# Performance work log

Hardware: AMD Instinct MI355X
Metric: run time of the kernel (lower is better)

The kernel has to match this reference:

```python
import jax, jax.numpy as jnp
import numpy as np
from jax import lax

B, S, H, T = 64, 512, 1024, 24


def setup_inputs() -> dict:
    key = jax.random.key(0)
    k1, k2, k3, k4, k5 = jax.random.split(key, 5)
    feats = jax.random.normal(k1, (B, S, H), dtype=jnp.float32)
    target = jax.random.randint(k2, (B, S), 0, T)  # tag ids (argmax of original one-hot target)
    # descending-sorted lengths -> prefix mask, matching the torch code's sorted-batch assumption
    lengths = jnp.sort(jax.random.randint(k3, (B,), S // 2, S + 1))[::-1]
    mask = jnp.arange(S)[None, :] < lengths[:, None]  # (B,S) bool
    # hidden2tag params (uniform init ~ nn.Linear default scale)
    bound = 1.0 / np.sqrt(H)
    W = jax.random.uniform(k4, (T, H), minval=-bound, maxval=bound, dtype=jnp.float32)
    b = jax.random.uniform(k5, (T,), minval=-bound, maxval=bound, dtype=jnp.float32)
    transition = jnp.zeros((T, T), dtype=jnp.float32)
    return {"feats": feats, "target": target, "mask": mask, "W": W, "b": b, "transition": transition}


def reference(feats, target, mask, W, b, transition):
    # emission scores: (B,S,T)
    emission = jnp.einsum("bsh,th->bst", feats, W) + b
    # gold path score
    sc = jnp.take_along_axis(emission, target[:, :, None], axis=2).squeeze(-1)  # (B,S)
    sc = sc.at[:, 1:].add(transition[target[:, :-1], target[:, 1:]])
    total_score = (sc * mask.astype(emission.dtype)).sum(axis=1)  # (B,)
    # forward algorithm (log-partition) as a scan over time
    p0 = emission[:, 0]  # (B,T)
    emis_t = jnp.swapaxes(emission[:, 1:], 0, 1)  # (S-1,B,T)
    mask_t = jnp.swapaxes(mask[:, 1:], 0, 1)      # (S-1,B)

    def step(p, xs):
        emit_i, m_i = xs
        # log_sum[b, prev, cur] = p[b, prev] + transition[prev, cur] + emit_i[b, cur]
        new_p = jax.nn.logsumexp(p[:, :, None] + transition[None, :, :] + emit_i[:, None, :], axis=1)
        return jnp.where(m_i[:, None], new_p, p), None

    p, _ = lax.scan(step, p0, (emis_t, mask_t))
    log_Z = jax.nn.logsumexp(p, axis=1)  # (B,)
    loss = -jnp.mean(total_score - log_Z)
    return loss, emission
```

## Files before the change

kernel.cpp:

```cpp
#include <hip/hip_runtime.h>
#include <cstdint>
#include <math.h>

#define B_ 64
#define S_ 512
#define H_ 1024
#define T_ 24
#define TP_ 32
#define NC_ 32
#define CL_ 16
#define KST_ 1040

typedef unsigned int u32;
typedef unsigned short u16;
typedef __attribute__((ext_vector_type(8))) short short8v;
typedef __attribute__((ext_vector_type(4))) float f32x4;
typedef __attribute__((ext_vector_type(4))) u32 uint4v;

__device__ __forceinline__ float rl_f32(float x, int sl) {
    return __uint_as_float(__builtin_amdgcn_readlane(__float_as_uint(x), sl));
}

__device__ __forceinline__ void split_pk(float f0, float f1, u32& hpk, u32& lpk) {
    const u32 u0 = __float_as_uint(f0), u1 = __float_as_uint(f1);
    const u32 t1 = u1 & 0xffff0000u;
    hpk = (u0 >> 16) | t1;
    const float fl0 = f0 - __uint_as_float(u0 & 0xffff0000u);
    const float fl1 = f1 - __uint_as_float(t1);
    lpk = (__float_as_uint(fl0) >> 16) | (__float_as_uint(fl1) & 0xffff0000u);
}

__global__ __launch_bounds__(256) void wcvt_kernel(const float* __restrict__ W,
                                                   u16* __restrict__ Wh,
                                                   u16* __restrict__ Wl,
                                                   float* __restrict__ out) {
    const int i = blockIdx.x * 256 + threadIdx.x;
    if (i == 0) out[0] = 0.f;
    const int t = i >> 10;
    const float f = (t < T_) ? W[i] : 0.f;
    const u32 u = __float_as_uint(f);
    const u32 rh = u + 0x7fffu + ((u >> 16) & 1u);
    const u16 hb = (u16)(rh >> 16);
    const float fh = __uint_as_float((u32)hb << 16);
    const float fl = f - fh;
    const u32 u2 = __float_as_uint(fl);
    const u32 rl2 = u2 + 0x7fffu + ((u2 >> 16) & 1u);
    Wh[i] = hb;
    Wl[i] = (u16)(rl2 >> 16);
}

__global__ __launch_bounds__(256) void gemm_kernel(const float* __restrict__ feats,
                                                   const u16* __restrict__ Wh,
                                                   const u16* __restrict__ Wl,
                                                   const float* __restrict__ bias,
                                                   float* __restrict__ emission) {
    const int tid  = threadIdx.x;
    const int lane = tid & 63;
    const int wv   = tid >> 6;
    const int r16  = lane & 15;
    const int g    = lane >> 4;
    const int mtile = blockIdx.x * 4 + wv;

    const float* ap  = feats + ((long)mtile * 16 + r16) * H_ + g * 8;
    const u16* bh0p = Wh + r16 * H_ + g * 8;
    const u16* bl0p = Wl + r16 * H_ + g * 8;
    const u16* bh1p = Wh + (r16 + 16) * H_ + g * 8;
    const u16* bl1p = Wl + (r16 + 16) * H_ + g * 8;

    f32x4 acc0 = {0.f, 0.f, 0.f, 0.f};
    f32x4 acc1 = {0.f, 0.f, 0.f, 0.f};

#pragma unroll 4
    for (int kk = 0; kk < H_ / 32; ++kk) {
        const int ko = kk * 32;
        const float4 a0 = *(const float4*)(ap + ko);
        const float4 a1 = *(const float4*)(ap + ko + 4);
        const short8v bh0 = *(const short8v*)(bh0p + ko);
        const short8v bl0 = *(const short8v*)(bl0p + ko);
        const short8v bh1 = *(const short8v*)(bh1p + ko);
        const short8v bl1 = *(const short8v*)(bl1p + ko);

        u32 h0, l0, h1, l1, h2, l2, h3, l3;
        split_pk(a0.x, a0.y, h0, l0);
        split_pk(a0.z, a0.w, h1, l1);
        split_pk(a1.x, a1.y, h2, l2);
        split_pk(a1.z, a1.w, h3, l3);
        const uint4v hv = {h0, h1, h2, h3};
        const uint4v lv = {l0, l1, l2, l3};
        const short8v ah = __builtin_bit_cast(short8v, hv);
        const short8v al = __builtin_bit_cast(short8v, lv);

        acc0 = __builtin_amdgcn_mfma_f32_16x16x32_bf16(al, bh0, acc0, 0, 0, 0);
        acc0 = __builtin_amdgcn_mfma_f32_16x16x32_bf16(ah, bl0, acc0, 0, 0, 0);
        acc0 = __builtin_amdgcn_mfma_f32_16x16x32_bf16(ah, bh0, acc0, 0, 0, 0);
        acc1 = __builtin_amdgcn_mfma_f32_16x16x32_bf16(al, bh1, acc1, 0, 0, 0);
        acc1 = __builtin_amdgcn_mfma_f32_16x16x32_bf16(ah, bl1, acc1, 0, 0, 0);
        acc1 = __builtin_amdgcn_mfma_f32_16x16x32_bf16(ah, bh1, acc1, 0, 0, 0);
    }

    const float b0 = bias[r16];
    const float b1 = (r16 + 16 < T_) ? bias[r16 + 16] : 0.f;
    float* op = emission + ((long)mtile * 16 + g * 4) * T_;
#pragma unroll
    for (int r = 0; r < 4; ++r) {
        op[r * T_ + r16] = acc0[r] + b0;
        if (r16 + 16 < T_) op[r * T_ + r16 + 16] = acc1[r] + b1;
    }
}

__global__ __launch_bounds__(64, 1) void chunk_kernel(const float* __restrict__ emission,
                                                      const int* __restrict__ mask,
                                                      const float* __restrict__ trans,
                                                      float* __restrict__ wsK) {
    __shared__ u32 lds[2][2][16][18];
    const int bid = blockIdx.x;
    const int c_ = bid & (NC_ - 1);
    const int b  = bid >> 5;
    const int l  = threadIdx.x;
    const int cc = l & 15;
    const int q  = l >> 4;
    const int aq4 = (l & 48);

    const float* em = emission + (long)b * S_ * T_;
    const int* mk = mask + b * S_;

    int mc = 0;
#pragma unroll
    for (int k = 0; k < 8; ++k) mc += mk[l + k * 64];
#pragma unroll
    for (int off = 32; off; off >>= 1) mc += __shfl_xor(mc, off);
    const int len = __builtin_amdgcn_readfirstlane(mc);

    const int lo = 1 + c_ * CL_;
    const int hi = min(lo + CL_, S_);
    const int send = min(hi, len);

    short8v Ah[2], Al[2];
#pragma unroll
    for (int I = 0; I < 2; ++I) {
        const int j = 16 * I + cc;
        u32 hw[4], lw[4];
#pragma unroll
        for (int w = 0; w < 4; ++w) {
            const int t0 = 8 * q + 2 * w;
            const float v0 = (t0 < 24 && j < 24) ? __expf(trans[t0 * T_ + j]) : 0.f;
            const float v1 = (t0 + 1 < 24 && j < 24) ? __expf(trans[(t0 + 1) * T_ + j]) : 0.f;
            split_pk(v0, v1, hw[w], lw[w]);
        }
        const uint4v hv = {hw[0], hw[1], hw[2], hw[3]};
        const uint4v lv = {lw[0], lw[1], lw[2], lw[3]};
        Ah[I] = __builtin_bit_cast(short8v, hv);
        Al[I] = __builtin_bit_cast(short8v, lv);
    }

    f32x4 K[2][2];
#pragma unroll
    for (int I = 0; I < 2; ++I)
#pragma unroll
        for (int J = 0; J < 2; ++J)
#pragma unroll
            for (int r = 0; r < 4; ++r)
                K[I][J][r] = (16 * I + 4 * q + r == 16 * J + cc) ? 1.f : 0.f;

    u32 bh[2][4], bl[2][4];
#pragma unroll
    for (int J = 0; J < 2; ++J)
#pragma unroll
        for (int w = 0; w < 4; ++w) {
            const int k0 = 8 * q + 2 * w, col = 16 * J + cc;
            bh[J][w] = (k0 == col ? 0x3f80u : 0u) | (k0 + 1 == col ? 0x3f800000u : 0u);
            bl[J][w] = 0u;
        }

    const int xj = ((l & 31) < 24) ? (l & 31) : 0;
    float xr_[CL_];
#pragma unroll
    for (int k = 0; k < CL_; ++k) {
        const int s = lo + k;
        xr_[k] = em[((s < S_) ? s : 0) * T_ + xj];
    }

    float Ls = 0.f;
    const f32x4 z4 = {0.f, 0.f, 0.f, 0.f};

#pragma unroll
    for (int k = 0; k < CL_; ++k) {
        const int s = lo + k;
        if (s < send) {
            const uint4v bh0v = {bh[0][0], bh[0][1], bh[0][2], bh[0][3]};
            const uint4v bh1v = {bh[1][0], bh[1][1], bh[1][2], bh[1][3]};
            const uint4v bl0v = {bl[0][0], bl[0][1], bl[0][2], bl[0][3]};
            const uint4v bl1v = {bl[1][0], bl[1][1], bl[1][2], bl[1][3]};
            const short8v B0h = __builtin_bit_cast(short8v, bh0v);
            const short8v B1h = __builtin_bit_cast(short8v, bh1v);
            const short8v B0l = __builtin_bit_cast(short8v, bl0v);
            const short8v B1l = __builtin_bit_cast(short8v, bl1v);

            f32x4 acc[2][2];
#pragma unroll
            for (int I = 0; I < 2; ++I) {
                acc[I][0] = __builtin_amdgcn_mfma_f32_16x16x32_bf16(Ah[I], B0h, z4, 0, 0, 0);
                acc[I][0] = __builtin_amdgcn_mfma_f32_16x16x32_bf16(Ah[I], B0l, acc[I][0], 0, 0, 0);
                acc[I][0] = __builtin_amdgcn_mfma_f32_16x16x32_bf16(Al[I], B0h, acc[I][0], 0, 0, 0);
                acc[I][1] = __builtin_amdgcn_mfma_f32_16x16x32_bf16(Ah[I], B1h, z4, 0, 0, 0);
                acc[I][1] = __builtin_amdgcn_mfma_f32_16x16x32_bf16(Ah[I], B1l, acc[I][1], 0, 0, 0);
                acc[I][1] = __builtin_amdgcn_mfma_f32_16x16x32_bf16(Al[I], B1h, acc[I][1], 0, 0, 0);
            }

            const float X = __expf(xr_[k]);
            const int xi = __float_as_int(X);
            float xr0[4], xr1[4];
#pragma unroll
            for (int r = 0; r < 4; ++r) {
                xr0[r] = __int_as_float(__builtin_amdgcn_ds_bpermute(aq4 + 4 * r, xi));
                xr1[r] = __int_as_float(__builtin_amdgcn_ds_bpermute(aq4 + 64 + 4 * r, xi));
            }
#pragma unroll
            for (int J = 0; J < 2; ++J)
#pragma unroll
                for (int r = 0; r < 4; ++r) {
                    K[0][J][r] = acc[0][J][r] * xr0[r];
                    K[1][J][r] = acc[1][J][r] * xr1[r];
                }

            if (k == 7 || k == CL_ - 1) {
                float mx = K[0][0][0];
#pragma unroll
                for (int I = 0; I < 2; ++I)
#pragma unroll
                    for (int J = 0; J < 2; ++J)
#pragma unroll
                        for (int r = 0; r < 4; ++r) mx = fmaxf(mx, K[I][J][r]);
#pragma unroll
                for (int off = 32; off; off >>= 1) mx = fmaxf(mx, __shfl_xor(mx, off));
                const u32 ef = __float_as_uint(mx) & 0x7f800000u;
                const float inv = __uint_as_float(0x7f000000u - ef);
#pragma unroll
                for (int I = 0; I < 2; ++I)
#pragma unroll
                    for (int J = 0; J < 2; ++J)
#pragma unroll
                        for (int r = 0; r < 4; ++r) K[I][J][r] *= inv;
                Ls += (float)((int)(ef >> 23) - 127) * 0.6931471805599453f;
            }

            if (k < CL_ - 1) {
#pragma unroll
                for (int I = 0; I < 2; ++I)
#pragma unroll
                    for (int J = 0; J < 2; ++J)
#pragma unroll
                        for (int m = 0; m < 2; ++m) {
                            u32 h, lo_w;
                            split_pk(K[I][J][2 * m], K[I][J][2 * m + 1], h, lo_w);
                            const int p = 8 * I + 2 * q + m;
                            lds[0][J][p][cc] = h;
                            lds[1][J][p][cc] = lo_w;
                        }
#pragma unroll
                for (int J = 0; J < 2; ++J)
#pragma unroll
                    for (int w = 0; w < 4; ++w) {
                        bh[J][w] = lds[0][J][4 * q + w][cc];
                        bl[J][w] = lds[1][J][4 * q + w][cc];
                    }
            }
        }
    }

    float* outp = wsK + (long)(b * NC_ + c_) * KST_;
#pragma unroll
    for (int I = 0; I < 2; ++I)
#pragma unroll
        for (int J = 0; J < 2; ++J)
#pragma unroll
            for (int r = 0; r < 4; ++r)
                outp[(16 * I + 4 * q + r) * 32 + 16 * J + cc] = K[I][J][r];
    if (l == 0) outp[1024] = Ls;
}

#define ACC4(kv, t0)                                                           \
    s0 = fmaf(rl_f32(p, (t0) + 0), kv.x, s0);                                  \
    s1 = fmaf(rl_f32(p, (t0) + 1), kv.y, s1);                                  \
    s2 = fmaf(rl_f32(p, (t0) + 2), kv.z, s2);                                  \
    s3 = fmaf(rl_f32(p, (t0) + 3), kv.w, s3);

__global__ __launch_bounds__(64) void finalize_kernel(const float* __restrict__ emission,
                                                      const int* __restrict__ target,
                                                      const int* __restrict__ mask,
                                                      const float* __restrict__ trans,
                                                      const float* __restrict__ wsK,
                                                      float* __restrict__ out) {
    const int b = blockIdx.x;
    const int j = threadIdx.x;
    const int jj = j < 24 ? j : 23;
    const float* em = emission + (long)b * S_ * T_;
    const int* mk = mask + b * S_;

    float p = (j < 24) ? __expf(em[j]) : 0.f;
    float C = 0.f;

    for (int c = 0; c < NC_; ++c) {
        const float* base = wsK + (long)(b * NC_ + c) * KST_;
        C += base[1024];
        const float4* rp = (const float4*)(base + jj * 32);
        const float4 k0 = rp[0], k1 = rp[1], k2 = rp[2], k3 = rp[3], k4 = rp[4], k5 = rp[5];
        float s0 = 0.f, s1 = 0.f, s2 = 0.f, s3 = 0.f;
        ACC4(k0, 0) ACC4(k1, 4) ACC4(k2, 8) ACC4(k3, 12) ACC4(k4, 16) ACC4(k5, 20)
        p = (j < 24) ? ((s0 + s1) + (s2 + s3)) : 0.f;
        float mx = p;
#pragma unroll
        for (int off = 32; off; off >>= 1) mx = fmaxf(mx, __shfl_xor(mx, off));
        const u32 ef = __float_as_uint(mx) & 0x7f800000u;
        p *= __uint_as_float(0x7f000000u - ef);
        C += (float)((int)(ef >> 23) - 127) * 0.6931471805599453f;
    }

    float ex = p;
#pragma unroll
    for (int off = 32; off; off >>= 1) ex += __shfl_down(ex, off);

    float ssum = 0.f;
#pragma unroll
    for (int kk = 0; kk < S_ / 64; ++kk) {
        const int s = j + kk * 64;
        if (mk[s]) {
            const int tg = target[b * S_ + s];
            float v = em[s * T_ + tg];
            if (s > 0) v += trans[target[b * S_ + s - 1] * T_ + tg];
            ssum += v;
        }
    }
#pragma unroll
    for (int off = 32; off; off >>= 1) ssum += __shfl_down(ssum, off);

    if (j == 0) {
        const float logZ = C + __logf(ex);
        atomicAdd(out, (logZ - ssum) * (1.0f / B_));
    }
}

extern "C" void kernel_launch(void* const* d_in, const int* in_sizes, int n_in,
                              void* d_out, int out_size, void* d_ws, size_t ws_size,
                              hipStream_t stream) {
    const float* feats  = (const float*)d_in[0];
    const int*   target = (const int*)d_in[1];
    const int*   mask   = (const int*)d_in[2];
    const float* W      = (const float*)d_in[3];
    const float* bias   = (const float*)d_in[4];
    const float* trans  = (const float*)d_in[5];

    float* out = (float*)d_out;
    float* emission = out + 1;
    u16* Wh = (u16*)d_ws;
    u16* Wl = Wh + TP_ * H_;
    float* wsK = (float*)((char*)d_ws + 131072);

    wcvt_kernel<<<(TP_ * H_) / 256, 256, 0, stream>>>(W, Wh, Wl, out);
    gemm_kernel<<<512, 256, 0, stream>>>(feats, Wh, Wl, bias, emission);
    chunk_kernel<<<B_ * NC_, 64, 0, stream>>>(emission, mask, trans, wsK);
    finalize_kernel<<<B_, 64, 0, stream>>>(emission, target, mask, trans, wsK, out);
}
```

Measured before the change: 260.0 us.

## Split GEMM K across waves and software-pipeline loads three stages deep

```diff
diff --git a/kernel.cpp b/kernel.cpp
--- a/kernel.cpp
+++ b/kernel.cpp
@@ -49,36 +49,62 @@
     Wl[i] = (u16)(rl2 >> 16);
 }
 
-__global__ __launch_bounds__(256) void gemm_kernel(const float* __restrict__ feats,
-                                                   const u16* __restrict__ Wh,
-                                                   const u16* __restrict__ Wl,
-                                                   const float* __restrict__ bias,
-                                                   float* __restrict__ emission) {
+__global__ __launch_bounds__(256, 4) void gemm_kernel(const float* __restrict__ feats,
+                                                      const u16* __restrict__ Wh,
+                                                      const u16* __restrict__ Wl,
+                                                      const float* __restrict__ bias,
+                                                      float* __restrict__ emission) {
+    __shared__ f32x4 ldsP[2][64][2];
     const int tid  = threadIdx.x;
     const int lane = tid & 63;
     const int wv   = tid >> 6;
+    const int mt_in = wv & 1;
+    const int kh    = wv >> 1;
     const int r16  = lane & 15;
     const int g    = lane >> 4;
-    const int mtile = blockIdx.x * 4 + wv;
-
-    const float* ap  = feats + ((long)mtile * 16 + r16) * H_ + g * 8;
-    const u16* bh0p = Wh + r16 * H_ + g * 8;
-    const u16* bl0p = Wl + r16 * H_ + g * 8;
-    const u16* bh1p = Wh + (r16 + 16) * H_ + g * 8;
-    const u16* bl1p = Wl + (r16 + 16) * H_ + g * 8;
+    const int mtile = blockIdx.x * 2 + mt_in;
+
+    const long ko0 = (long)kh * 512 + g * 8;
+    const float* ap  = feats + ((long)mtile * 16 + r16) * H_ + ko0;
+    const u16* bh0p = Wh + r16 * H_ + ko0;
+    const u16* bl0p = Wl + r16 * H_ + ko0;
+    const u16* bh1p = Wh + (r16 + 16) * H_ + ko0;
+    const u16* bl1p = Wl + (r16 + 16) * H_ + ko0;
 
     f32x4 acc0 = {0.f, 0.f, 0.f, 0.f};
     f32x4 acc1 = {0.f, 0.f, 0.f, 0.f};
 
-#pragma unroll 4
-    for (int kk = 0; kk < H_ / 32; ++kk) {
-        const int ko = kk * 32;
-        const float4 a0 = *(const float4*)(ap + ko);
-        const float4 a1 = *(const float4*)(ap + ko + 4);
-        const short8v bh0 = *(const short8v*)(bh0p + ko);
-        const short8v bl0 = *(const short8v*)(bl0p + ko);
-        const short8v bh1 = *(const short8v*)(bh1p + ko);
-        const short8v bl1 = *(const short8v*)(bl1p + ko);
+    float4 A0[3], A1[3];
+    short8v BH0[3], BL0[3], BH1[3], BL1[3];
+#pragma unroll
+    for (int p = 0; p < 3; ++p) {
+        const int ko = p * 32;
+        A0[p]  = *(const float4*)(ap + ko);
+        A1[p]  = *(const float4*)(ap + ko + 4);
+        BH0[p] = *(const short8v*)(bh0p + ko);
+        BL0[p] = *(const short8v*)(bl0p + ko);
+        BH1[p] = *(const short8v*)(bh1p + ko);
+        BL1[p] = *(const short8v*)(bl1p + ko);
+    }
+
+#pragma unroll
+    for (int kk = 0; kk < 16; ++kk) {
+        const int sl = kk % 3;
+        const float4 a0 = A0[sl];
+        const float4 a1 = A1[sl];
+        const short8v bh0 = BH0[sl];
+        const short8v bl0 = BL0[sl];
+        const short8v bh1 = BH1[sl];
+        const short8v bl1 = BL1[sl];
+        if (kk + 3 < 16) {
+            const int ko = (kk + 3) * 32;
+            A0[sl]  = *(const float4*)(ap + ko);
+            A1[sl]  = *(const float4*)(ap + ko + 4);
+            BH0[sl] = *(const short8v*)(bh0p + ko);
+            BL0[sl] = *(const short8v*)(bl0p + ko);
+            BH1[sl] = *(const short8v*)(bh1p + ko);
+            BL1[sl] = *(const short8v*)(bl1p + ko);
+        }
 
         u32 h0, l0, h1, l1, h2, l2, h3, l3;
         split_pk(a0.x, a0.y, h0, l0);
@@ -98,13 +124,27 @@
         acc1 = __builtin_amdgcn_mfma_f32_16x16x32_bf16(ah, bh1, acc1, 0, 0, 0);
     }
 
-    const float b0 = bias[r16];
-    const float b1 = (r16 + 16 < T_) ? bias[r16 + 16] : 0.f;
-    float* op = emission + ((long)mtile * 16 + g * 4) * T_;
-#pragma unroll
-    for (int r = 0; r < 4; ++r) {
-        op[r * T_ + r16] = acc0[r] + b0;
-        if (r16 + 16 < T_) op[r * T_ + r16 + 16] = acc1[r] + b1;
+    if (kh == 1) {
+        ldsP[mt_in][lane][0] = acc0;
+        ldsP[mt_in][lane][1] = acc1;
+    }
+    __syncthreads();
+    if (kh == 0) {
+        const f32x4 p0 = ldsP[mt_in][lane][0];
+        const f32x4 p1 = ldsP[mt_in][lane][1];
+#pragma unroll
+        for (int r = 0; r < 4; ++r) {
+            acc0[r] += p0[r];
+            acc1[r] += p1[r];
+        }
+        const float b0 = bias[r16];
+        const float b1 = (r16 + 16 < T_) ? bias[r16 + 16] : 0.f;
+        float* op = emission + ((long)mtile * 16 + g * 4) * T_;
+#pragma unroll
+        for (int r = 0; r < 4; ++r) {
+            op[r * T_ + r16] = acc0[r] + b0;
+            if (r16 + 16 < T_) op[r * T_ + r16 + 16] = acc1[r] + b1;
+        }
     }
 }
 
@@ -357,7 +397,7 @@
     float* wsK = (float*)((char*)d_ws + 131072);
 
     wcvt_kernel<<<(TP_ * H_) / 256, 256, 0, stream>>>(W, Wh, Wl, out);
-    gemm_kernel<<<512, 256, 0, stream>>>(feats, Wh, Wl, bias, emission);
+    gemm_kernel<<<1024, 256, 0, stream>>>(feats, Wh, Wl, bias, emission);
     chunk_kernel<<<B_ * NC_, 64, 0, stream>>>(emission, mask, trans, wsK);
     finalize_kernel<<<B_, 64, 0, stream>>>(emission, target, mask, trans, wsK, out);
 }
```

Result: no change. 259.0 us (-0.4%).

## Fuse emission GEMM, chunk scan and finalize into one kernel

Applied to the files above, without the earlier changes.

```diff
diff --git a/kernel.cpp b/kernel.cpp
--- a/kernel.cpp
+++ b/kernel.cpp
@@ -33,9 +33,11 @@
 __global__ __launch_bounds__(256) void wcvt_kernel(const float* __restrict__ W,
                                                    u16* __restrict__ Wh,
                                                    u16* __restrict__ Wl,
-                                                   float* __restrict__ out) {
+                                                   float* __restrict__ out,
+                                                   int* __restrict__ cnt) {
     const int i = blockIdx.x * 256 + threadIdx.x;
     if (i == 0) out[0] = 0.f;
+    if (i < B_) cnt[i] = 0;
     const int t = i >> 10;
     const float f = (t < T_) ? W[i] : 0.f;
     const u32 u = __float_as_uint(f);
@@ -49,70 +51,22 @@
     Wl[i] = (u16)(rl2 >> 16);
 }
 
-__global__ __launch_bounds__(256) void gemm_kernel(const float* __restrict__ feats,
-                                                   const u16* __restrict__ Wh,
-                                                   const u16* __restrict__ Wl,
-                                                   const float* __restrict__ bias,
-                                                   float* __restrict__ emission) {
-    const int tid  = threadIdx.x;
-    const int lane = tid & 63;
-    const int wv   = tid >> 6;
-    const int r16  = lane & 15;
-    const int g    = lane >> 4;
-    const int mtile = blockIdx.x * 4 + wv;
-
-    const float* ap  = feats + ((long)mtile * 16 + r16) * H_ + g * 8;
-    const u16* bh0p = Wh + r16 * H_ + g * 8;
-    const u16* bl0p = Wl + r16 * H_ + g * 8;
-    const u16* bh1p = Wh + (r16 + 16) * H_ + g * 8;
-    const u16* bl1p = Wl + (r16 + 16) * H_ + g * 8;
-
-    f32x4 acc0 = {0.f, 0.f, 0.f, 0.f};
-    f32x4 acc1 = {0.f, 0.f, 0.f, 0.f};
-
-#pragma unroll 4
-    for (int kk = 0; kk < H_ / 32; ++kk) {
-        const int ko = kk * 32;
-        const float4 a0 = *(const float4*)(ap + ko);
-        const float4 a1 = *(const float4*)(ap + ko + 4);
-        const short8v bh0 = *(const short8v*)(bh0p + ko);
-        const short8v bl0 = *(const short8v*)(bl0p + ko);
-        const short8v bh1 = *(const short8v*)(bh1p + ko);
-        const short8v bl1 = *(const short8v*)(bl1p + ko);
-
-        u32 h0, l0, h1, l1, h2, l2, h3, l3;
-        split_pk(a0.x, a0.y, h0, l0);
-        split_pk(a0.z, a0.w, h1, l1);
-        split_pk(a1.x, a1.y, h2, l2);
-        split_pk(a1.z, a1.w, h3, l3);
-        const uint4v hv = {h0, h1, h2, h3};
-        const uint4v lv = {l0, l1, l2, l3};
-        const short8v ah = __builtin_bit_cast(short8v, hv);
-        const short8v al = __builtin_bit_cast(short8v, lv);
-
-        acc0 = __builtin_amdgcn_mfma_f32_16x16x32_bf16(al, bh0, acc0, 0, 0, 0);
-        acc0 = __builtin_amdgcn_mfma_f32_16x16x32_bf16(ah, bl0, acc0, 0, 0, 0);
-        acc0 = __builtin_amdgcn_mfma_f32_16x16x32_bf16(ah, bh0, acc0, 0, 0, 0);
-        acc1 = __builtin_amdgcn_mfma_f32_16x16x32_bf16(al, bh1, acc1, 0, 0, 0);
-        acc1 = __builtin_amdgcn_mfma_f32_16x16x32_bf16(ah, bl1, acc1, 0, 0, 0);
-        acc1 = __builtin_amdgcn_mfma_f32_16x16x32_bf16(ah, bh1, acc1, 0, 0, 0);
-    }
-
-    const float b0 = bias[r16];
-    const float b1 = (r16 + 16 < T_) ? bias[r16 + 16] : 0.f;
-    float* op = emission + ((long)mtile * 16 + g * 4) * T_;
-#pragma unroll
-    for (int r = 0; r < 4; ++r) {
-        op[r * T_ + r16] = acc0[r] + b0;
-        if (r16 + 16 < T_) op[r * T_ + r16 + 16] = acc1[r] + b1;
-    }
-}
-
-__global__ __launch_bounds__(64, 1) void chunk_kernel(const float* __restrict__ emission,
+#define FINE_DECL(i) const float E##i##_ = 0.f; (void)E##i##_;
+
+__global__ __launch_bounds__(64, 1) void fused_kernel(const float* __restrict__ feats,
+                                                      const u16* __restrict__ Wh,
+                                                      const u16* __restrict__ Wl,
+                                                      const float* __restrict__ bias,
+                                                      const float* __restrict__ trans,
+                                                      const int* __restrict__ target,
                                                       const int* __restrict__ mask,
-                                                      const float* __restrict__ trans,
-                                                      float* __restrict__ wsK) {
+                                                      float* __restrict__ emission,
+                                                      float* __restrict__ wsK,
+                                                      int* __restrict__ cnt,
+                                                      float* __restrict__ out) {
+    __shared__ float em_lds[16][32];
     __shared__ u32 lds[2][2][16][18];
+
     const int bid = blockIdx.x;
     const int c_ = bid & (NC_ - 1);
     const int b  = bid >> 5;
@@ -124,6 +78,59 @@
     const float* em = emission + (long)b * S_ * T_;
     const int* mk = mask + b * S_;
 
+    {
+        const long row0 = (long)b * S_ + 16 * c_;
+        const float* ap  = feats + (row0 + cc) * H_ + q * 8;
+        const u16* bh0p = Wh + cc * H_ + q * 8;
+        const u16* bl0p = Wl + cc * H_ + q * 8;
+        const u16* bh1p = Wh + (cc + 16) * H_ + q * 8;
+        const u16* bl1p = Wl + (cc + 16) * H_ + q * 8;
+
+        f32x4 acc0 = {0.f, 0.f, 0.f, 0.f};
+        f32x4 acc1 = {0.f, 0.f, 0.f, 0.f};
+
+#pragma unroll 4
+        for (int kk = 0; kk < H_ / 32; ++kk) {
+            const int ko = kk * 32;
+            const float4 a0 = *(const float4*)(ap + ko);
+            const float4 a1 = *(const float4*)(ap + ko + 4);
+            const short8v bh0 = *(const short8v*)(bh0p + ko);
+            const short8v bl0 = *(const short8v*)(bl0p + ko);
+            const short8v bh1 = *(const short8v*)(bh1p + ko);
+            const short8v bl1 = *(const short8v*)(bl1p + ko);
+
+            u32 h0, l0, h1, l1, h2, l2, h3, l3;
+            split_pk(a0.x, a0.y, h0, l0);
+            split_pk(a0.z, a0.w, h1, l1);
+            split_pk(a1.x, a1.y, h2, l2);
+            split_pk(a1.z, a1.w, h3, l3);
+            const uint4v hv = {h0, h1, h2, h3};
+            const uint4v lv = {l0, l1, l2, l3};
+            const short8v ah = __builtin_bit_cast(short8v, hv);
+            const short8v al = __builtin_bit_cast(short8v, lv);
+
+            acc0 = __builtin_amdgcn_mfma_f32_16x16x32_bf16(al, bh0, acc0, 0, 0, 0);
+            acc0 = __builtin_amdgcn_mfma_f32_16x16x32_bf16(ah, bl0, acc0, 0, 0, 0);
+            acc0 = __builtin_amdgcn_mfma_f32_16x16x32_bf16(ah, bh0, acc0, 0, 0, 0);
+            acc1 = __builtin_amdgcn_mfma_f32_16x16x32_bf16(al, bh1, acc1, 0, 0, 0);
+            acc1 = __builtin_amdgcn_mfma_f32_16x16x32_bf16(ah, bl1, acc1, 0, 0, 0);
+            acc1 = __builtin_amdgcn_mfma_f32_16x16x32_bf16(ah, bh1, acc1, 0, 0, 0);
+        }
+
+        const float b0 = bias[cc];
+        const float b1 = (cc + 16 < T_) ? bias[cc + 16] : 0.f;
+#pragma unroll
+        for (int r = 0; r < 4; ++r) {
+            const float e0 = acc0[r] + b0;
+            const float e1 = acc1[r] + b1;
+            em_lds[4 * q + r][cc] = e0;
+            em_lds[4 * q + r][16 + cc] = e1;
+            float* op = emission + (row0 + 4 * q + r) * T_;
+            op[cc] = e0;
+            if (cc + 16 < T_) op[16 + cc] = e1;
+        }
+    }
+
     int mc = 0;
 #pragma unroll
     for (int k = 0; k < 8; ++k) mc += mk[l + k * 64];
@@ -131,9 +138,8 @@
     for (int off = 32; off; off >>= 1) mc += __shfl_xor(mc, off);
     const int len = __builtin_amdgcn_readfirstlane(mc);
 
-    const int lo = 1 + c_ * CL_;
-    const int hi = min(lo + CL_, S_);
-    const int send = min(hi, len);
+    const int s0_ = 16 * c_;
+    const int send = min(s0_ + CL_, len);
 
     short8v Ah[2], Al[2];
 #pragma unroll
@@ -172,21 +178,13 @@
             bl[J][w] = 0u;
         }
 
-    const int xj = ((l & 31) < 24) ? (l & 31) : 0;
-    float xr_[CL_];
-#pragma unroll
-    for (int k = 0; k < CL_; ++k) {
-        const int s = lo + k;
-        xr_[k] = em[((s < S_) ? s : 0) * T_ + xj];
-    }
-
     float Ls = 0.f;
     const f32x4 z4 = {0.f, 0.f, 0.f, 0.f};
 
 #pragma unroll
     for (int k = 0; k < CL_; ++k) {
-        const int s = lo + k;
-        if (s < send) {
+        const int s = s0_ + k;
+        if (s > 0 && s < send) {
             const uint4v bh0v = {bh[0][0], bh[0][1], bh[0][2], bh[0][3]};
             const uint4v bh1v = {bh[1][0], bh[1][1], bh[1][2], bh[1][3]};
             const uint4v bl0v = {bl[0][0], bl[0][1], bl[0][2], bl[0][3]};
@@ -207,7 +205,7 @@
                 acc[I][1] = __builtin_amdgcn_mfma_f32_16x16x32_bf16(Al[I], B1h, acc[I][1], 0, 0, 0);
             }
 
-            const float X = __expf(xr_[k]);
+            const float X = __expf(em_lds[k][l & 31]);
             const int xi = __float_as_int(X);
             float xr0[4], xr1[4];
 #pragma unroll
@@ -277,26 +275,16 @@
             for (int r = 0; r < 4; ++r)
                 outp[(16 * I + 4 * q + r) * 32 + 16 * J + cc] = K[I][J][r];
     if (l == 0) outp[1024] = Ls;
-}
-
-#define ACC4(kv, t0)                                                           \
-    s0 = fmaf(rl_f32(p, (t0) + 0), kv.x, s0);                                  \
-    s1 = fmaf(rl_f32(p, (t0) + 1), kv.y, s1);                                  \
-    s2 = fmaf(rl_f32(p, (t0) + 2), kv.z, s2);                                  \
-    s3 = fmaf(rl_f32(p, (t0) + 3), kv.w, s3);
-
-__global__ __launch_bounds__(64) void finalize_kernel(const float* __restrict__ emission,
-                                                      const int* __restrict__ target,
-                                                      const int* __restrict__ mask,
-                                                      const float* __restrict__ trans,
-                                                      const float* __restrict__ wsK,
-                                                      float* __restrict__ out) {
-    const int b = blockIdx.x;
-    const int j = threadIdx.x;
+
+    __threadfence();
+    int myprev = 0;
+    if (l == 0) myprev = atomicAdd(cnt + b, 1);
+    myprev = __shfl(myprev, 0);
+    if (myprev != NC_ - 1) return;
+    __threadfence();
+
+    const int j = l;
     const int jj = j < 24 ? j : 23;
-    const float* em = emission + (long)b * S_ * T_;
-    const int* mk = mask + b * S_;
-
     float p = (j < 24) ? __expf(em[j]) : 0.f;
     float C = 0.f;
 
@@ -306,7 +294,13 @@
         const float4* rp = (const float4*)(base + jj * 32);
         const float4 k0 = rp[0], k1 = rp[1], k2 = rp[2], k3 = rp[3], k4 = rp[4], k5 = rp[5];
         float s0 = 0.f, s1 = 0.f, s2 = 0.f, s3 = 0.f;
+#define ACC4(kv, t0)                                                           \
+        s0 = fmaf(rl_f32(p, (t0) + 0), kv.x, s0);                              \
+        s1 = fmaf(rl_f32(p, (t0) + 1), kv.y, s1);                              \
+        s2 = fmaf(rl_f32(p, (t0) + 2), kv.z, s2);                              \
+        s3 = fmaf(rl_f32(p, (t0) + 3), kv.w, s3);
         ACC4(k0, 0) ACC4(k1, 4) ACC4(k2, 8) ACC4(k3, 12) ACC4(k4, 16) ACC4(k5, 20)
+#undef ACC4
         p = (j < 24) ? ((s0 + s1) + (s2 + s3)) : 0.f;
         float mx = p;
 #pragma unroll
@@ -355,9 +349,9 @@
     u16* Wh = (u16*)d_ws;
     u16* Wl = Wh + TP_ * H_;
     float* wsK = (float*)((char*)d_ws + 131072);
-
-    wcvt_kernel<<<(TP_ * H_) / 256, 256, 0, stream>>>(W, Wh, Wl, out);
-    gemm_kernel<<<512, 256, 0, stream>>>(feats, Wh, Wl, bias, emission);
-    chunk_kernel<<<B_ * NC_, 64, 0, stream>>>(emission, mask, trans, wsK);
-    finalize_kernel<<<B_, 64, 0, stream>>>(emission, target, mask, trans, wsK, out);
-}
+    int* cnt = (int*)((char*)d_ws + 131072 + (size_t)B_ * NC_ * KST_ * 4);
+
+    wcvt_kernel<<<(TP_ * H_) / 256, 256, 0, stream>>>(W, Wh, Wl, out, cnt);
+    fused_kernel<<<B_ * NC_, 64, 0, stream>>>(feats, Wh, Wl, bias, trans, target, mask,
+                                              emission, wsK, cnt, out);
+}
```

Measured after the change: 343.2 us. 32.0% more time.

## Stage GEMM feats through LDS with register double-buffering; prefetch finalize chunks

Applied to the files above, without the earlier changes.

```diff
diff --git a/kernel.cpp b/kernel.cpp
--- a/kernel.cpp
+++ b/kernel.cpp
@@ -49,58 +49,97 @@
     Wl[i] = (u16)(rl2 >> 16);
 }
 
-__global__ __launch_bounds__(256) void gemm_kernel(const float* __restrict__ feats,
-                                                   const u16* __restrict__ Wh,
-                                                   const u16* __restrict__ Wl,
-                                                   const float* __restrict__ bias,
-                                                   float* __restrict__ emission) {
+__global__ __launch_bounds__(256, 2) void gemm_kernel(const float* __restrict__ feats,
+                                                      const u16* __restrict__ Wh,
+                                                      const u16* __restrict__ Wl,
+                                                      const float* __restrict__ bias,
+                                                      float* __restrict__ emission) {
+    __shared__ float2 A2[4][16][33];
     const int tid  = threadIdx.x;
     const int lane = tid & 63;
-    const int wv   = tid >> 6;
+    const int w    = tid >> 6;
     const int r16  = lane & 15;
     const int g    = lane >> 4;
-    const int mtile = blockIdx.x * 4 + wv;
-
-    const float* ap  = feats + ((long)mtile * 16 + r16) * H_ + g * 8;
-    const u16* bh0p = Wh + r16 * H_ + g * 8;
-    const u16* bl0p = Wl + r16 * H_ + g * 8;
-    const u16* bh1p = Wh + (r16 + 16) * H_ + g * 8;
-    const u16* bl1p = Wl + (r16 + 16) * H_ + g * 8;
+    const int mtile = blockIdx.x * 4 + w;
+    const long row0 = (long)mtile * 16;
+
+    const int srow  = lane >> 4;
+    const int sslot = lane & 15;
+
+    const float* fb = feats + row0 * H_;
+    const u16* bh0p = Wh + r16 * H_;
+    const u16* bl0p = Wl + r16 * H_;
+    const u16* bh1p = Wh + (r16 + 16) * H_;
+    const u16* bl1p = Wl + (r16 + 16) * H_;
 
     f32x4 acc0 = {0.f, 0.f, 0.f, 0.f};
     f32x4 acc1 = {0.f, 0.f, 0.f, 0.f};
 
-#pragma unroll 4
-    for (int kk = 0; kk < H_ / 32; ++kk) {
-        const int ko = kk * 32;
-        const float4 a0 = *(const float4*)(ap + ko);
-        const float4 a1 = *(const float4*)(ap + ko + 4);
-        const short8v bh0 = *(const short8v*)(bh0p + ko);
-        const short8v bl0 = *(const short8v*)(bl0p + ko);
-        const short8v bh1 = *(const short8v*)(bh1p + ko);
-        const short8v bl1 = *(const short8v*)(bl1p + ko);
-
-        u32 h0, l0, h1, l1, h2, l2, h3, l3;
-        split_pk(a0.x, a0.y, h0, l0);
-        split_pk(a0.z, a0.w, h1, l1);
-        split_pk(a1.x, a1.y, h2, l2);
-        split_pk(a1.z, a1.w, h3, l3);
-        const uint4v hv = {h0, h1, h2, h3};
-        const uint4v lv = {l0, l1, l2, l3};
-        const short8v ah = __builtin_bit_cast(short8v, hv);
-        const short8v al = __builtin_bit_cast(short8v, lv);
-
-        acc0 = __builtin_amdgcn_mfma_f32_16x16x32_bf16(al, bh0, acc0, 0, 0, 0);
-        acc0 = __builtin_amdgcn_mfma_f32_16x16x32_bf16(ah, bl0, acc0, 0, 0, 0);
-        acc0 = __builtin_amdgcn_mfma_f32_16x16x32_bf16(ah, bh0, acc0, 0, 0, 0);
-        acc1 = __builtin_amdgcn_mfma_f32_16x16x32_bf16(al, bh1, acc1, 0, 0, 0);
-        acc1 = __builtin_amdgcn_mfma_f32_16x16x32_bf16(ah, bl1, acc1, 0, 0, 0);
-        acc1 = __builtin_amdgcn_mfma_f32_16x16x32_bf16(ah, bh1, acc1, 0, 0, 0);
-    }
+    float4 rgA[4], rgB[4];
+
+#define LOADCH(rg, c)                                                          \
+    do {                                                                       \
+        _Pragma("unroll") for (int i = 0; i < 4; ++i)                          \
+            rg[i] = *(const float4*)(fb + (long)(4 * i + srow) * H_ +          \
+                                     (c) * 64 + sslot * 4);                    \
+    } while (0)
+
+#define WRITECH(rg)                                                            \
+    do {                                                                       \
+        _Pragma("unroll") for (int i = 0; i < 4; ++i) {                        \
+            A2[w][4 * i + srow][sslot * 2]     = make_float2(rg[i].x, rg[i].y);\
+            A2[w][4 * i + srow][sslot * 2 + 1] = make_float2(rg[i].z, rg[i].w);\
+        }                                                                      \
+    } while (0)
+
+#define COMPCH(c)                                                              \
+    do {                                                                       \
+        _Pragma("unroll") for (int t = 0; t < 2; ++t) {                        \
+            const float2 f0 = A2[w][r16][16 * t + 4 * g + 0];                  \
+            const float2 f1 = A2[w][r16][16 * t + 4 * g + 1];                  \
+            const float2 f2 = A2[w][r16][16 * t + 4 * g + 2];                  \
+            const float2 f3 = A2[w][r16][16 * t + 4 * g + 3];                  \
+            const int ko = (c) * 64 + t * 32 + g * 8;                          \
+            const short8v bh0 = *(const short8v*)(bh0p + ko);                  \
+            const short8v bl0 = *(const short8v*)(bl0p + ko);                  \
+            const short8v bh1 = *(const short8v*)(bh1p + ko);                  \
+            const short8v bl1 = *(const short8v*)(bl1p + ko);                  \
+            u32 h0, l0, h1, l1, h2, l2, h3, l3;                                \
+            split_pk(f0.x, f0.y, h0, l0);                                      \
+            split_pk(f1.x, f1.y, h1, l1);                                      \
+            split_pk(f2.x, f2.y, h2, l2);                                      \
+            split_pk(f3.x, f3.y, h3, l3);                                      \
+            const uint4v hv = {h0, h1, h2, h3};                                \
+            const uint4v lv = {l0, l1, l2, l3};                                \
+            const short8v ah = __builtin_bit_cast(short8v, hv);                \
+            const short8v al = __builtin_bit_cast(short8v, lv);                \
+            acc0 = __builtin_amdgcn_mfma_f32_16x16x32_bf16(al, bh0, acc0, 0, 0, 0); \
+            acc0 = __builtin_amdgcn_mfma_f32_16x16x32_bf16(ah, bl0, acc0, 0, 0, 0); \
+            acc0 = __builtin_amdgcn_mfma_f32_16x16x32_bf16(ah, bh0, acc0, 0, 0, 0); \
+            acc1 = __builtin_amdgcn_mfma_f32_16x16x32_bf16(al, bh1, acc1, 0, 0, 0); \
+            acc1 = __builtin_amdgcn_mfma_f32_16x16x32_bf16(ah, bl1, acc1, 0, 0, 0); \
+            acc1 = __builtin_amdgcn_mfma_f32_16x16x32_bf16(ah, bh1, acc1, 0, 0, 0); \
+        }                                                                      \
+    } while (0)
+
+    LOADCH(rgA, 0);
+    LOADCH(rgB, 1);
+#pragma unroll
+    for (int c = 0; c < 16; c += 2) {
+        WRITECH(rgA);
+        if (c + 2 < 16) LOADCH(rgA, c + 2);
+        COMPCH(c);
+        WRITECH(rgB);
+        if (c + 3 < 16) LOADCH(rgB, c + 3);
+        COMPCH(c + 1);
+    }
+#undef LOADCH
+#undef WRITECH
+#undef COMPCH
 
     const float b0 = bias[r16];
     const float b1 = (r16 + 16 < T_) ? bias[r16 + 16] : 0.f;
-    float* op = emission + ((long)mtile * 16 + g * 4) * T_;
+    float* op = emission + (row0 + g * 4) * T_;
 #pragma unroll
     for (int r = 0; r < 4; ++r) {
         op[r * T_ + r16] = acc0[r] + b0;
@@ -300,20 +339,33 @@
     float p = (j < 24) ? __expf(em[j]) : 0.f;
     float C = 0.f;
 
+    const float* base = wsK + (long)b * NC_ * KST_;
+
+    const float4* rp0 = (const float4*)(base + jj * 32);
+    float4 n0 = rp0[0], n1 = rp0[1], n2 = rp0[2], n3 = rp0[3], n4 = rp0[4], n5 = rp0[5];
+    float nL = base[1024];
+
     for (int c = 0; c < NC_; ++c) {
-        const float* base = wsK + (long)(b * NC_ + c) * KST_;
-        C += base[1024];
-        const float4* rp = (const float4*)(base + jj * 32);
-        const float4 k0 = rp[0], k1 = rp[1], k2 = rp[2], k3 = rp[3], k4 = rp[4], k5 = rp[5];
+        const float4 k0 = n0, k1 = n1, k2 = n2, k3 = n3, k4 = n4, k5 = n5;
+        const float L = nL;
+        if (c + 1 < NC_) {
+            const float* nb = base + (long)(c + 1) * KST_;
+            const float4* np = (const float4*)(nb + jj * 32);
+            n0 = np[0]; n1 = np[1]; n2 = np[2]; n3 = np[3]; n4 = np[4]; n5 = np[5];
+            nL = nb[1024];
+        }
+        C += L;
         float s0 = 0.f, s1 = 0.f, s2 = 0.f, s3 = 0.f;
         ACC4(k0, 0) ACC4(k1, 4) ACC4(k2, 8) ACC4(k3, 12) ACC4(k4, 16) ACC4(k5, 20)
         p = (j < 24) ? ((s0 + s1) + (s2 + s3)) : 0.f;
-        float mx = p;
-#pragma unroll
-        for (int off = 32; off; off >>= 1) mx = fmaxf(mx, __shfl_xor(mx, off));
-        const u32 ef = __float_as_uint(mx) & 0x7f800000u;
-        p *= __uint_as_float(0x7f000000u - ef);
-        C += (float)((int)(ef >> 23) - 127) * 0.6931471805599453f;
+        if ((c & 1) || c == NC_ - 1) {
+            float mx = p;
+#pragma unroll
+            for (int off = 32; off; off >>= 1) mx = fmaxf(mx, __shfl_xor(mx, off));
+            const u32 ef = __float_as_uint(mx) & 0x7f800000u;
+            p *= __uint_as_float(0x7f000000u - ef);
+            C += (float)((int)(ef >> 23) - 127) * 0.6931471805599453f;
+        }
     }
 
     float ex = p;
```

Result: no change. 265.1 us (+1.9%).
